# Kernel optimization log

Measured on AMD Instinct MI355X. Metric: run time of the kernel, lower is better.

Reference implementation:

```python
import jax, jax.numpy as jnp
import numpy as np

N_NODES = 50000
BETA = 0.5
NEG_SLOPE = 0.2


def gat_conv(x, src, dst, W, a_src, a_dst, b):
    """Single-head GAT-style conv: gather, attend, softmax-per-dst, scatter-sum."""
    h = x @ W                                   # [N, F]
    as_ = h @ a_src                             # [N]
    ad_ = h @ a_dst                             # [N]
    e = jax.nn.leaky_relu(as_[src] + ad_[dst], NEG_SLOPE)  # [E]
    # numerically stable softmax over incoming edges of each dst node
    m = jax.ops.segment_max(e, dst, num_segments=N_NODES)  # [N]
    ex = jnp.exp(e - m[dst])                    # [E]
    denom = jax.ops.segment_sum(ex, dst, num_segments=N_NODES)  # [N]
    w = ex / denom[dst]                         # [E]
    out = jax.ops.segment_sum(w[:, None] * h[src], dst, num_segments=N_NODES)
    return out + b


def setup_inputs() -> dict:
    key = jax.random.key(0)
    ks = jax.random.split(key, 8)
    F_in, F_out = 64, 64
    x = jax.random.normal(ks[0], (N_NODES, F_in), dtype=jnp.float32)
    edge_index = jax.random.randint(ks[1], (2, 1600000), 0, N_NODES, dtype=jnp.int64)
    W = jax.random.normal(ks[2], (F_in, F_in), dtype=jnp.float32) * (1.0 / np.sqrt(F_in))
    a_src = jax.random.normal(ks[3], (F_in,), dtype=jnp.float32) * (1.0 / np.sqrt(F_in))
    a_dst = jax.random.normal(ks[4], (F_in,), dtype=jnp.float32) * (1.0 / np.sqrt(F_in))
    b = jnp.zeros((F_in,), dtype=jnp.float32)
    fc_w = jax.random.normal(ks[5], (F_in, F_out), dtype=jnp.float32) * (1.0 / np.sqrt(F_in))
    fc_b = jnp.zeros((F_out,), dtype=jnp.float32)
    return {"x": x, "edge_index": edge_index, "W": W, "a_src": a_src,
            "a_dst": a_dst, "b": b, "fc_w": fc_w, "fc_b": fc_b}


def reference(x, edge_index, W, a_src, a_dst, b, fc_w, fc_b):
    src, dst = edge_index[0], edge_index[1]
    x1 = BETA * gat_conv(x, src, dst, W, a_src, a_dst, b) + (1.0 - BETA) * x
    x2 = BETA * gat_conv(x1, src, dst, W, a_src, a_dst, b) + (1.0 - BETA) * x
    x3 = BETA * gat_conv(x2, src, dst, W, a_src, a_dst, b) + (1.0 - BETA) * x
    h = x3
    out = x3 @ fc_w + fc_b
    return (out, h)
```

## Files before the change

kernel.cpp:

```cpp
#include <hip/hip_runtime.h>
#include <hip/hip_bf16.h>
#include <math.h>

#define N_NODES 50000
#define FDIM 64
#define BETA 0.5f
#define NEG_SLOPE 0.2f

typedef __attribute__((ext_vector_type(8))) short bf16x8;
typedef __attribute__((ext_vector_type(4))) float f32x4;

__device__ __forceinline__ unsigned short f2bf(float f) {
    unsigned u = __float_as_uint(f);
    unsigned r = (u + 0x7FFFu + ((u >> 16) & 1u)) >> 16;
    return (unsigned short)r;
}
__device__ __forceinline__ float bf2f(unsigned short s) {
    return __uint_as_float((unsigned)s << 16);
}

__global__ void detect_kernel(const unsigned int* __restrict__ ei, int* flag, int nCheck) {
    int i = blockIdx.x * blockDim.x + threadIdx.x;
    if (i < nCheck) {
        if (ei[2 * i + 1] != 0u) atomicOr(flag, 1);
    }
}

__global__ __launch_bounds__(256) void hist_kernel(
    const int* __restrict__ ei32, const long long* __restrict__ ei64,
    const int* __restrict__ flag, int* __restrict__ bucketCounts, int E) {
    __shared__ int h[256];
    int t = threadIdx.x;
    h[t] = 0;
    __syncthreads();
    bool is32 = (*flag) != 0;
    for (int i = blockIdx.x * blockDim.x + t; i < E; i += gridDim.x * blockDim.x) {
        int d = is32 ? ei32[E + i] : (int)ei64[E + i];
        atomicAdd(&h[d >> 8], 1);
    }
    __syncthreads();
    if (h[t]) atomicAdd(&bucketCounts[t], h[t]);
}

__global__ __launch_bounds__(256) void bucket_scan(
    const int* __restrict__ bucketCounts, int* __restrict__ bucketOffsets,
    int* __restrict__ bucketCursor, int* __restrict__ offsets, int NB, int N, int E) {
    __shared__ int sc[256];
    int t = threadIdx.x;
    int c = (t < NB) ? bucketCounts[t] : 0;
    sc[t] = c;
    __syncthreads();
    for (int off = 1; off < 256; off <<= 1) {
        int v = (t >= off) ? sc[t - off] : 0;
        __syncthreads();
        sc[t] += v;
        __syncthreads();
    }
    int excl = sc[t] - c;
    if (t < NB) { bucketOffsets[t] = excl; bucketCursor[t] = excl; }
    if (t == NB - 1) bucketOffsets[NB] = excl + c;
    if (t == 0) offsets[N] = E;
}

#define CHUNK 4096
__global__ __launch_bounds__(256) void scatter_pairs(
    const int* __restrict__ ei32, const long long* __restrict__ ei64,
    const int* __restrict__ flag, int* __restrict__ bucketCursor,
    unsigned int* __restrict__ pairs, int E) {
    __shared__ int hist[256], base[256], cur[256];
    int t = threadIdx.x;
    hist[t] = 0; cur[t] = 0;
    __syncthreads();
    int beg = blockIdx.x * CHUNK;
    int end = min(E, beg + CHUNK);
    bool is32 = (*flag) != 0;
    for (int i = beg + t; i < end; i += 256) {
        int d = is32 ? ei32[E + i] : (int)ei64[E + i];
        atomicAdd(&hist[d >> 8], 1);
    }
    __syncthreads();
    if (hist[t] > 0) base[t] = atomicAdd(&bucketCursor[t], hist[t]);
    __syncthreads();
    for (int i = beg + t; i < end; i += 256) {
        int s, d;
        if (is32) { s = ei32[i]; d = ei32[E + i]; }
        else      { s = (int)ei64[i]; d = (int)ei64[E + i]; }
        int b = d >> 8;
        int pos = base[b] + atomicAdd(&cur[b], 1);
        pairs[pos] = (unsigned int)s | ((unsigned int)(d & 255) << 16);
    }
}

__global__ __launch_bounds__(256) void bucket_sort(
    const unsigned int* __restrict__ pairs, const int* __restrict__ bucketOffsets,
    int* __restrict__ offsets, int* __restrict__ srcs, int N) {
    __shared__ int cnt[256], sc[256], cur[256];
    int b = blockIdx.x, t = threadIdx.x;
    int beg = bucketOffsets[b], end = bucketOffsets[b + 1];
    cnt[t] = 0;
    __syncthreads();
    for (int i = beg + t; i < end; i += 256) atomicAdd(&cnt[(pairs[i] >> 16) & 255u], 1);
    __syncthreads();
    sc[t] = cnt[t];
    __syncthreads();
    for (int off = 1; off < 256; off <<= 1) {
        int v = (t >= off) ? sc[t - off] : 0;
        __syncthreads();
        sc[t] += v;
        __syncthreads();
    }
    int excl = sc[t] - cnt[t];
    int node = (b << 8) + t;
    if (node < N) offsets[node] = beg + excl;
    cur[t] = beg + excl;
    __syncthreads();
    for (int i = beg + t; i < end; i += 256) {
        unsigned int p = pairs[i];
        int pos = atomicAdd(&cur[(p >> 16) & 255u], 1);
        srcs[pos] = (int)(p & 0xFFFFu);
    }
}

__global__ __launch_bounds__(256) void prep_weights(
    const float* __restrict__ W, const float* __restrict__ fcw,
    unsigned short* __restrict__ WTh, unsigned short* __restrict__ WTl,
    unsigned short* __restrict__ FTh, unsigned short* __restrict__ FTl) {
    for (int idx = blockIdx.x * 256 + threadIdx.x; idx < 4096; idx += gridDim.x * 256) {
        int k = idx >> 6, f = idx & 63;
        float w = W[idx];
        unsigned short hi = f2bf(w);
        WTh[f * 64 + k] = hi;
        WTl[f * 64 + k] = f2bf(w - bf2f(hi));
        float w2 = fcw[idx];
        unsigned short hi2 = f2bf(w2);
        FTh[f * 64 + k] = hi2;
        FTl[f * 64 + k] = f2bf(w2 - bf2f(hi2));
    }
}

__global__ __launch_bounds__(256, 4) void transform_mfma(
    const float* __restrict__ x,
    const unsigned short* __restrict__ WTh, const unsigned short* __restrict__ WTl,
    const float* __restrict__ a_src, const float* __restrict__ a_dst,
    const float* __restrict__ bias,
    unsigned short* __restrict__ hb,
    float* __restrict__ fout,
    float* __restrict__ as_, float* __restrict__ ad_, int N) {
    __shared__ __align__(16) unsigned short WThs[64 * 72];
    __shared__ __align__(16) unsigned short WTls[64 * 72];
    int tid = threadIdx.x;
    {
        int row = tid >> 2;
        int ch = (tid & 3) * 16;
        uint4 h0 = ((const uint4*)(WTh + row * 64 + ch))[0];
        uint4 h1 = ((const uint4*)(WTh + row * 64 + ch))[1];
        uint4 l0 = ((const uint4*)(WTl + row * 64 + ch))[0];
        uint4 l1 = ((const uint4*)(WTl + row * 64 + ch))[1];
        *((uint4*)(WThs + row * 72 + ch)) = h0;
        *((uint4*)(WThs + row * 72 + ch + 8)) = h1;
        *((uint4*)(WTls + row * 72 + ch)) = l0;
        *((uint4*)(WTls + row * 72 + ch + 8)) = l1;
    }

    int wid = tid >> 6;
    int lane = tid & 63;
    int col = lane & 15;
    int quad = lane >> 4;
    int mbase = blockIdx.x * 64 + wid * 16;

    bf16x8 Ah[2], Al[2];
    int arow = mbase + col;
    const float* xr = x + (size_t)(arow < N ? arow : 0) * FDIM + quad * 8;
#pragma unroll
    for (int ks = 0; ks < 2; ks++) {
        float4 xa = *(const float4*)(xr + ks * 32);
        float4 xb = *(const float4*)(xr + ks * 32 + 4);
        float xv[8] = {xa.x, xa.y, xa.z, xa.w, xb.x, xb.y, xb.z, xb.w};
#pragma unroll
        for (int e = 0; e < 8; e++) {
            unsigned short hi = f2bf(xv[e]);
            Ah[ks][e] = (short)hi;
            Al[ks][e] = (short)f2bf(xv[e] - bf2f(hi));
        }
    }
    __syncthreads();

    f32x4 acc[4];
#pragma unroll
    for (int ft = 0; ft < 4; ft++) acc[ft] = (f32x4){0.f, 0.f, 0.f, 0.f};

#pragma unroll
    for (int ft = 0; ft < 4; ft++) {
        int f = ft * 16 + col;
#pragma unroll
        for (int ks = 0; ks < 2; ks++) {
            int off = f * 72 + ks * 32 + quad * 8;
            bf16x8 Bh = *(const bf16x8*)(WThs + off);
            bf16x8 Bl = *(const bf16x8*)(WTls + off);
            acc[ft] = __builtin_amdgcn_mfma_f32_16x16x32_bf16(Ah[ks], Bh, acc[ft], 0, 0, 0);
            acc[ft] = __builtin_amdgcn_mfma_f32_16x16x32_bf16(Ah[ks], Bl, acc[ft], 0, 0, 0);
            acc[ft] = __builtin_amdgcn_mfma_f32_16x16x32_bf16(Al[ks], Bh, acc[ft], 0, 0, 0);
        }
    }

    if (fout) {
#pragma unroll
        for (int ft = 0; ft < 4; ft++) {
            int f = ft * 16 + col;
            float bv = bias ? bias[f] : 0.f;
#pragma unroll
            for (int r = 0; r < 4; r++) {
                int node = mbase + quad * 4 + r;
                if (node < N) fout[(size_t)node * FDIM + f] = acc[ft][r] + bv;
            }
        }
    }
    if (hb) {
#pragma unroll
        for (int ft = 0; ft < 4; ft++) {
            int f = ft * 16 + col;
#pragma unroll
            for (int r = 0; r < 4; r++) {
                int node = mbase + quad * 4 + r;
                if (node < N) hb[(size_t)node * FDIM + f] = f2bf(acc[ft][r]);
            }
        }
    }
    if (as_) {
        float asv[4], adv[4];
#pragma unroll
        for (int ft = 0; ft < 4; ft++) {
            asv[ft] = a_src[ft * 16 + col];
            adv[ft] = a_dst[ft * 16 + col];
        }
#pragma unroll
        for (int r = 0; r < 4; r++) {
            float pa = 0.f, pd = 0.f;
#pragma unroll
            for (int ft = 0; ft < 4; ft++) {
                pa = fmaf(acc[ft][r], asv[ft], pa);
                pd = fmaf(acc[ft][r], adv[ft], pd);
            }
#pragma unroll
            for (int off = 1; off <= 8; off <<= 1) {
                pa += __shfl_xor(pa, off, 64);
                pd += __shfl_xor(pd, off, 64);
            }
            int node = mbase + quad * 4 + r;
            if (col == 0 && node < N) { as_[node] = pa; ad_[node] = pd; }
        }
    }
}

__global__ __launch_bounds__(256) void gat_gather(
    const unsigned short* __restrict__ hb,
    const float* __restrict__ as_, const float* __restrict__ ad_,
    const int* __restrict__ offsets, const int* __restrict__ srcs,
    const float* __restrict__ bvec, const float* __restrict__ x0,
    float* __restrict__ xout, int N) {
    int wid = (blockIdx.x * blockDim.x + threadIdx.x) >> 6;
    if (wid >= N) return;
    int lane = threadIdx.x & 63;
    int g = lane >> 4;
    int q = lane & 15;
    int beg = offsets[wid], end = offsets[wid + 1];
    float adv = ad_[wid];

    float4 acc = {0.f, 0.f, 0.f, 0.f};
    float denom = 0.f;
    const unsigned short* hq = hb + (q << 2);

#define SLOT(J)                                                              \
    {                                                                        \
        int j_ = (J);                                                        \
        float exj = __shfl(ex, j_, 64);                                      \
        int sj = __shfl(s, j_, 64);                                          \
        ushort4 hv = *(const ushort4*)(hq + (size_t)sj * FDIM);              \
        acc.x = fmaf(exj, bf2f(hv.x), acc.x);                                \
        acc.y = fmaf(exj, bf2f(hv.y), acc.y);                                \
        acc.z = fmaf(exj, bf2f(hv.z), acc.z);                                \
        acc.w = fmaf(exj, bf2f(hv.w), acc.w);                                \
    }

    for (int cbeg = beg; cbeg < end; cbeg += 64) {
        int i = cbeg + lane;
        float ex = 0.f;
        int s = 0;
        if (i < end) {
            s = srcs[i];
            float e = as_[s] + adv;
            e = e > 0.f ? e : NEG_SLOPE * e;
            ex = __expf(e);
        }
        denom += ex;
        int cnt = min(64, end - cbeg);
        int njj = (cnt + 3) >> 2;
        int jj = 0;
        for (; jj + 4 <= njj; jj += 4) {
            int j0 = (jj << 2) | g;
            SLOT(j0); SLOT(j0 + 4); SLOT(j0 + 8); SLOT(j0 + 12);
        }
        for (; jj < njj; jj++) {
            SLOT((jj << 2) | g);
        }
    }
#undef SLOT

#pragma unroll
    for (int off = 32; off; off >>= 1) denom += __shfl_xor(denom, off, 64);
#pragma unroll
    for (int off = 16; off <= 32; off <<= 1) {
        acc.x += __shfl_xor(acc.x, off, 64);
        acc.y += __shfl_xor(acc.y, off, 64);
        acc.z += __shfl_xor(acc.z, off, 64);
        acc.w += __shfl_xor(acc.w, off, 64);
    }
    if (g == 0) {
        float inv = denom > 0.f ? 1.f / denom : 0.f;
        float4 b4 = *(const float4*)(bvec + (q << 2));
        float4 xv = *(const float4*)(x0 + (size_t)wid * FDIM + (q << 2));
        float4 o;
        o.x = BETA * (acc.x * inv + b4.x) + (1.f - BETA) * xv.x;
        o.y = BETA * (acc.y * inv + b4.y) + (1.f - BETA) * xv.y;
        o.z = BETA * (acc.z * inv + b4.z) + (1.f - BETA) * xv.z;
        o.w = BETA * (acc.w * inv + b4.w) + (1.f - BETA) * xv.w;
        *(float4*)(xout + (size_t)wid * FDIM + (q << 2)) = o;
    }
}

extern "C" void kernel_launch(void* const* d_in, const int* in_sizes, int n_in,
                              void* d_out, int out_size, void* d_ws, size_t ws_size,
                              hipStream_t stream) {
    const int N = N_NODES;
    const int E = in_sizes[1] / 2;
    const int NB = (N + 255) >> 8;

    const float* x     = (const float*)d_in[0];
    const void*  ei    = d_in[1];
    const float* W     = (const float*)d_in[2];
    const float* a_src = (const float*)d_in[3];
    const float* a_dst = (const float*)d_in[4];
    const float* bvec  = (const float*)d_in[5];
    const float* fc_w  = (const float*)d_in[6];
    const float* fc_b  = (const float*)d_in[7];

    float* out = (float*)d_out;
    float* x3  = out + (size_t)N * FDIM;

    char* p = (char*)d_ws;
    auto alloc = [&](size_t bytes) -> void* {
        void* r = (void*)p;
        p += (bytes + 255) & ~(size_t)255;
        return r;
    };
    int*            flag     = (int*)alloc(256);
    int*            bCounts  = (int*)alloc(256 * 4);
    int*            bOffsets = (int*)alloc(257 * 4);
    int*            bCursor  = (int*)alloc(256 * 4);
    unsigned int*   pairs    = (unsigned int*)alloc((size_t)E * 4);
    int*            srcs     = (int*)alloc((size_t)E * 4);
    int*            offsets  = (int*)alloc((size_t)(N + 1) * 4);
    float*          as_      = (float*)alloc((size_t)N * 4);
    float*          ad_      = (float*)alloc((size_t)N * 4);
    unsigned short* hbuf     = (unsigned short*)alloc((size_t)N * FDIM * 2);
    float*          xbuf     = (float*)alloc((size_t)N * FDIM * 4);
    unsigned short* WTh      = (unsigned short*)alloc(4096 * 2);
    unsigned short* WTl      = (unsigned short*)alloc(4096 * 2);
    unsigned short* FTh      = (unsigned short*)alloc(4096 * 2);
    unsigned short* FTl      = (unsigned short*)alloc(4096 * 2);

    hipMemsetAsync(flag, 0, 4, stream);
    hipMemsetAsync(bCounts, 0, 256 * 4, stream);

    const int nCheck = 65536;
    detect_kernel<<<nCheck / 256, 256, 0, stream>>>((const unsigned int*)ei, flag, nCheck);

    prep_weights<<<16, 256, 0, stream>>>(W, fc_w, WTh, WTl, FTh, FTl);

    hist_kernel<<<512, 256, 0, stream>>>((const int*)ei, (const long long*)ei, flag, bCounts, E);
    bucket_scan<<<1, 256, 0, stream>>>(bCounts, bOffsets, bCursor, offsets, NB, N, E);
    scatter_pairs<<<(E + CHUNK - 1) / CHUNK, 256, 0, stream>>>(
        (const int*)ei, (const long long*)ei, flag, bCursor, pairs, E);
    bucket_sort<<<NB, 256, 0, stream>>>(pairs, bOffsets, offsets, srcs, N);

    int tgrid = (N + 63) / 64;
    int ggrid = (N * 64 + 255) / 256;

    transform_mfma<<<tgrid, 256, 0, stream>>>(x, WTh, WTl, a_src, a_dst, nullptr,
                                              hbuf, nullptr, as_, ad_, N);
    gat_gather<<<ggrid, 256, 0, stream>>>(hbuf, as_, ad_, offsets, srcs, bvec, x, xbuf, N);
    transform_mfma<<<tgrid, 256, 0, stream>>>(xbuf, WTh, WTl, a_src, a_dst, nullptr,
                                              hbuf, nullptr, as_, ad_, N);
    gat_gather<<<ggrid, 256, 0, stream>>>(hbuf, as_, ad_, offsets, srcs, bvec, x, xbuf, N);
    transform_mfma<<<tgrid, 256, 0, stream>>>(xbuf, WTh, WTl, a_src, a_dst, nullptr,
                                              hbuf, nullptr, as_, ad_, N);
    gat_gather<<<ggrid, 256, 0, stream>>>(hbuf, as_, ad_, offsets, srcs, bvec, x, x3, N);
    transform_mfma<<<tgrid, 256, 0, stream>>>(x3, FTh, FTl, nullptr, nullptr, fc_b,
                                              nullptr, out, nullptr, nullptr, N);
}
```

Measured before the change: 295.2 us.

## Split bf16 features into two planes and drop separate detect/scan kernels

Stores the bf16 transformed features as two 32-feature planes so each gather block works on one half of the features. Consecutive block pairs process the same destination nodes on different planes, which is meant to shrink the per-plane gather footprint and improve cache locality. The index-width detection and bucket scan are folded into the histogram, scatter and sort kernels, removing two launches and one memset. The trade-offs are that softmax scores are now recomputed twice per edge, and every block redundantly recomputes the 256-entry scan. Nontemporal loads and stores are added for streaming data.

Result: slower. 352.2 us (+19.3%).

```diff
diff --git a/kernel.cpp b/kernel.cpp
--- a/kernel.cpp
+++ b/kernel.cpp
@@ -19,21 +19,19 @@
     return __uint_as_float((unsigned)s << 16);
 }
 
-__global__ void detect_kernel(const unsigned int* __restrict__ ei, int* flag, int nCheck) {
-    int i = blockIdx.x * blockDim.x + threadIdx.x;
-    if (i < nCheck) {
-        if (ei[2 * i + 1] != 0u) atomicOr(flag, 1);
-    }
-}
-
 __global__ __launch_bounds__(256) void hist_kernel(
-    const int* __restrict__ ei32, const long long* __restrict__ ei64,
-    const int* __restrict__ flag, int* __restrict__ bucketCounts, int E) {
+    const unsigned int* __restrict__ eiu, const int* __restrict__ ei32,
+    const long long* __restrict__ ei64, int* __restrict__ bucketCounts, int E) {
+    __shared__ int det;
     __shared__ int h[256];
     int t = threadIdx.x;
+    if (t == 0) det = 0;
     h[t] = 0;
     __syncthreads();
-    bool is32 = (*flag) != 0;
+    unsigned base = blockIdx.x * 256 + t;
+    if (base < (unsigned)E && eiu[2 * base + 1] != 0u) atomicOr(&det, 1);
+    __syncthreads();
+    bool is32 = det != 0;
     for (int i = blockIdx.x * blockDim.x + t; i < E; i += gridDim.x * blockDim.x) {
         int d = is32 ? ei32[E + i] : (int)ei64[E + i];
         atomicAdd(&h[d >> 8], 1);
@@ -42,44 +40,40 @@
     if (h[t]) atomicAdd(&bucketCounts[t], h[t]);
 }
 
-__global__ __launch_bounds__(256) void bucket_scan(
-    const int* __restrict__ bucketCounts, int* __restrict__ bucketOffsets,
-    int* __restrict__ bucketCursor, int* __restrict__ offsets, int NB, int N, int E) {
-    __shared__ int sc[256];
+#define CHUNK 4096
+__global__ __launch_bounds__(256) void scatter_pairs(
+    const unsigned int* __restrict__ eiu, const int* __restrict__ ei32,
+    const long long* __restrict__ ei64, const int* __restrict__ bucketCounts,
+    int* __restrict__ gCursor, unsigned int* __restrict__ pairs, int E) {
+    __shared__ int det;
+    __shared__ int sc[256], hist[256], base[256], cur[256];
     int t = threadIdx.x;
-    int c = (t < NB) ? bucketCounts[t] : 0;
+    if (t == 0) det = 0;
+    hist[t] = 0; cur[t] = 0;
+    __syncthreads();
+    int beg = blockIdx.x * CHUNK;
+    int end = min(E, beg + CHUNK);
+    {
+        int idx = beg + t;
+        if (idx < E && eiu[2 * idx + 1] != 0u) atomicOr(&det, 1);
+    }
+    int c = bucketCounts[t];
     sc[t] = c;
     __syncthreads();
+    bool is32 = det != 0;
     for (int off = 1; off < 256; off <<= 1) {
         int v = (t >= off) ? sc[t - off] : 0;
         __syncthreads();
         sc[t] += v;
         __syncthreads();
     }
-    int excl = sc[t] - c;
-    if (t < NB) { bucketOffsets[t] = excl; bucketCursor[t] = excl; }
-    if (t == NB - 1) bucketOffsets[NB] = excl + c;
-    if (t == 0) offsets[N] = E;
-}
-
-#define CHUNK 4096
-__global__ __launch_bounds__(256) void scatter_pairs(
-    const int* __restrict__ ei32, const long long* __restrict__ ei64,
-    const int* __restrict__ flag, int* __restrict__ bucketCursor,
-    unsigned int* __restrict__ pairs, int E) {
-    __shared__ int hist[256], base[256], cur[256];
-    int t = threadIdx.x;
-    hist[t] = 0; cur[t] = 0;
-    __syncthreads();
-    int beg = blockIdx.x * CHUNK;
-    int end = min(E, beg + CHUNK);
-    bool is32 = (*flag) != 0;
+    int bucketExcl = sc[t] - c;
     for (int i = beg + t; i < end; i += 256) {
         int d = is32 ? ei32[E + i] : (int)ei64[E + i];
         atomicAdd(&hist[d >> 8], 1);
     }
     __syncthreads();
-    if (hist[t] > 0) base[t] = atomicAdd(&bucketCursor[t], hist[t]);
+    if (hist[t] > 0) base[t] = bucketExcl + atomicAdd(&gCursor[t], hist[t]);
     __syncthreads();
     for (int i = beg + t; i < end; i += 256) {
         int s, d;
@@ -92,11 +86,22 @@
 }
 
 __global__ __launch_bounds__(256) void bucket_sort(
-    const unsigned int* __restrict__ pairs, const int* __restrict__ bucketOffsets,
-    int* __restrict__ offsets, int* __restrict__ srcs, int N) {
-    __shared__ int cnt[256], sc[256], cur[256];
+    const unsigned int* __restrict__ pairs, const int* __restrict__ bucketCounts,
+    int* __restrict__ offsets, int* __restrict__ srcs, int N, int E) {
+    __shared__ int scb[256], cnt[256], sc[256], cur[256];
     int b = blockIdx.x, t = threadIdx.x;
-    int beg = bucketOffsets[b], end = bucketOffsets[b + 1];
+    int cb = bucketCounts[t];
+    scb[t] = cb;
+    __syncthreads();
+    for (int off = 1; off < 256; off <<= 1) {
+        int v = (t >= off) ? scb[t - off] : 0;
+        __syncthreads();
+        scb[t] += v;
+        __syncthreads();
+    }
+    int beg = scb[b] - bucketCounts[b];
+    int end = scb[b];
+    if (b == 0 && t == 0) offsets[N] = E;
     cnt[t] = 0;
     __syncthreads();
     for (int i = beg + t; i < end; i += 256) atomicAdd(&cnt[(pairs[i] >> 16) & 255u], 1);
@@ -219,10 +224,12 @@
 #pragma unroll
         for (int ft = 0; ft < 4; ft++) {
             int f = ft * 16 + col;
+            size_t pb = (size_t)(f >> 5) * N;
+            int fo = f & 31;
 #pragma unroll
             for (int r = 0; r < 4; r++) {
                 int node = mbase + quad * 4 + r;
-                if (node < N) hb[(size_t)node * FDIM + f] = f2bf(acc[ft][r]);
+                if (node < N) hb[(pb + node) * 32 + fo] = f2bf(acc[ft][r]);
             }
         }
     }
@@ -258,24 +265,27 @@
     const int* __restrict__ offsets, const int* __restrict__ srcs,
     const float* __restrict__ bvec, const float* __restrict__ x0,
     float* __restrict__ xout, int N) {
-    int wid = (blockIdx.x * blockDim.x + threadIdx.x) >> 6;
-    if (wid >= N) return;
+    int b = blockIdx.x;
+    int plane = (b >> 2) & 1;
+    int w = (b >> 3) * 4 + (b & 3);
+    int dst = w * 4 + (threadIdx.x >> 6);
+    if (dst >= N) return;
     int lane = threadIdx.x & 63;
-    int g = lane >> 4;
-    int q = lane & 15;
-    int beg = offsets[wid], end = offsets[wid + 1];
-    float adv = ad_[wid];
-
-    float4 acc = {0.f, 0.f, 0.f, 0.f};
+    int eslot = lane >> 3;
+    int q = lane & 7;
+    int beg = offsets[dst], end = offsets[dst + 1];
+    float adv = ad_[dst];
+
+    f32x4 acc = {0.f, 0.f, 0.f, 0.f};
     float denom = 0.f;
-    const unsigned short* hq = hb + (q << 2);
+    const unsigned short* hq = hb + (size_t)plane * N * 32 + (q << 2);
 
 #define SLOT(J)                                                              \
     {                                                                        \
         int j_ = (J);                                                        \
         float exj = __shfl(ex, j_, 64);                                      \
         int sj = __shfl(s, j_, 64);                                          \
-        ushort4 hv = *(const ushort4*)(hq + (size_t)sj * FDIM);              \
+        ushort4 hv = *(const ushort4*)(hq + (size_t)sj * 32);                \
         acc.x = fmaf(exj, bf2f(hv.x), acc.x);                                \
         acc.y = fmaf(exj, bf2f(hv.y), acc.y);                                \
         acc.z = fmaf(exj, bf2f(hv.z), acc.z);                                \
@@ -287,21 +297,21 @@
         float ex = 0.f;
         int s = 0;
         if (i < end) {
-            s = srcs[i];
+            s = __builtin_nontemporal_load(&srcs[i]);
             float e = as_[s] + adv;
             e = e > 0.f ? e : NEG_SLOPE * e;
             ex = __expf(e);
         }
         denom += ex;
         int cnt = min(64, end - cbeg);
-        int njj = (cnt + 3) >> 2;
+        int njj = (cnt + 7) >> 3;
         int jj = 0;
         for (; jj + 4 <= njj; jj += 4) {
-            int j0 = (jj << 2) | g;
-            SLOT(j0); SLOT(j0 + 4); SLOT(j0 + 8); SLOT(j0 + 12);
+            int j0 = (jj << 3) | eslot;
+            SLOT(j0); SLOT(j0 + 8); SLOT(j0 + 16); SLOT(j0 + 24);
         }
         for (; jj < njj; jj++) {
-            SLOT((jj << 2) | g);
+            SLOT((jj << 3) | eslot);
         }
     }
 #undef SLOT
@@ -309,22 +319,24 @@
 #pragma unroll
     for (int off = 32; off; off >>= 1) denom += __shfl_xor(denom, off, 64);
 #pragma unroll
-    for (int off = 16; off <= 32; off <<= 1) {
+    for (int off = 8; off <= 32; off <<= 1) {
         acc.x += __shfl_xor(acc.x, off, 64);
         acc.y += __shfl_xor(acc.y, off, 64);
         acc.z += __shfl_xor(acc.z, off, 64);
         acc.w += __shfl_xor(acc.w, off, 64);
     }
-    if (g == 0) {
+    if (eslot == 0) {
         float inv = denom > 0.f ? 1.f / denom : 0.f;
-        float4 b4 = *(const float4*)(bvec + (q << 2));
-        float4 xv = *(const float4*)(x0 + (size_t)wid * FDIM + (q << 2));
-        float4 o;
+        int fbase = plane * 32 + (q << 2);
+        const f32x4* b4p = (const f32x4*)(bvec + fbase);
+        f32x4 b4 = *b4p;
+        f32x4 xv = __builtin_nontemporal_load((const f32x4*)(x0 + (size_t)dst * FDIM + fbase));
+        f32x4 o;
         o.x = BETA * (acc.x * inv + b4.x) + (1.f - BETA) * xv.x;
         o.y = BETA * (acc.y * inv + b4.y) + (1.f - BETA) * xv.y;
         o.z = BETA * (acc.z * inv + b4.z) + (1.f - BETA) * xv.z;
         o.w = BETA * (acc.w * inv + b4.w) + (1.f - BETA) * xv.w;
-        *(float4*)(xout + (size_t)wid * FDIM + (q << 2)) = o;
+        __builtin_nontemporal_store(o, (f32x4*)(xout + (size_t)dst * FDIM + fbase));
     }
 }
 
@@ -353,10 +365,7 @@
         p += (bytes + 255) & ~(size_t)255;
         return r;
     };
-    int*            flag     = (int*)alloc(256);
-    int*            bCounts  = (int*)alloc(256 * 4);
-    int*            bOffsets = (int*)alloc(257 * 4);
-    int*            bCursor  = (int*)alloc(256 * 4);
+    int*            bCounts  = (int*)alloc(512 * 4);
     unsigned int*   pairs    = (unsigned int*)alloc((size_t)E * 4);
     int*            srcs     = (int*)alloc((size_t)E * 4);
     int*            offsets  = (int*)alloc((size_t)(N + 1) * 4);
@@ -368,23 +377,21 @@
     unsigned short* WTl      = (unsigned short*)alloc(4096 * 2);
     unsigned short* FTh      = (unsigned short*)alloc(4096 * 2);
     unsigned short* FTl      = (unsigned short*)alloc(4096 * 2);
-
-    hipMemsetAsync(flag, 0, 4, stream);
-    hipMemsetAsync(bCounts, 0, 256 * 4, stream);
-
-    const int nCheck = 65536;
-    detect_kernel<<<nCheck / 256, 256, 0, stream>>>((const unsigned int*)ei, flag, nCheck);
+    int* gCursor = bCounts + 256;
+
+    hipMemsetAsync(bCounts, 0, 512 * 4, stream);
 
     prep_weights<<<16, 256, 0, stream>>>(W, fc_w, WTh, WTl, FTh, FTl);
 
-    hist_kernel<<<512, 256, 0, stream>>>((const int*)ei, (const long long*)ei, flag, bCounts, E);
-    bucket_scan<<<1, 256, 0, stream>>>(bCounts, bOffsets, bCursor, offsets, NB, N, E);
+    hist_kernel<<<512, 256, 0, stream>>>((const unsigned int*)ei, (const int*)ei,
+                                         (const long long*)ei, bCounts, E);
     scatter_pairs<<<(E + CHUNK - 1) / CHUNK, 256, 0, stream>>>(
-        (const int*)ei, (const long long*)ei, flag, bCursor, pairs, E);
-    bucket_sort<<<NB, 256, 0, stream>>>(pairs, bOffsets, offsets, srcs, N);
+        (const unsigned int*)ei, (const int*)ei, (const long long*)ei,
+        bCounts, gCursor, pairs, E);
+    bucket_sort<<<NB, 256, 0, stream>>>(pairs, bCounts, offsets, srcs, N, E);
 
     int tgrid = (N + 63) / 64;
-    int ggrid = (N * 64 + 255) / 256;
+    int ggrid = 2 * ((N + 3) / 4);
 
     transform_mfma<<<tgrid, 256, 0, stream>>>(x, WTh, WTl, a_src, a_dst, nullptr,
                                               hbuf, nullptr, as_, ad_, N);
```
